# Performance work log

Measured on AMD Instinct MI355X. Metric: run time of the kernel, lower is better.

Reference implementation:

```python
import jax, jax.numpy as jnp
import numpy as np

B, O, E, H = 8192, 256, 64, 4  # batch, num_orbital, num_electron, hidden size


def setup_inputs() -> dict:
    key = jax.random.key(0)
    kx, k1, k2, k3, k4, k5, k6 = jax.random.split(key, 7)
    # occupancy vector: exactly E ones per sample among O orbitals
    perm_keys = jax.random.split(kx, B)
    occ = jax.vmap(lambda k: jax.random.permutation(k, O)[:E])(perm_keys)  # [B, E]
    x = jnp.zeros((B, O), jnp.float32).at[jnp.arange(B)[:, None], occ].set(1.0)
    # hidden Dense layers (kernel_init = uniform[0, 0.2), bias = zeros, as in flax default bias)
    W1 = jax.random.uniform(k1, (O, H), jnp.float32, 0.0, 0.2)
    b1 = jnp.zeros((H,), jnp.float32)
    W2 = jax.random.uniform(k2, (H, H), jnp.float32, 0.0, 0.2)
    b2 = jnp.zeros((H,), jnp.float32)
    # DenseGeneral: H -> (O, E); lecun_normal-ish init
    Wg = jax.random.normal(k3, (H, O, E), jnp.float32) / jnp.sqrt(jnp.float32(H))
    bg = jnp.zeros((O, E), jnp.float32)
    return {"x": x, "W1": W1, "b1": b1, "W2": W2, "b2": b2, "Wg": Wg, "bg": bg}


def reference(x, W1, b1, W2, b2, Wg, bg):
    # occupied orbital indices, ascending, fixed size E (vmapped jnp.nonzero)
    sel = jax.vmap(lambda row: jnp.nonzero(row, size=E, fill_value=0)[0])(x)  # [B, E] int
    # tiny MLP
    h = jax.nn.relu(x @ W1 + b1)        # [B, H]
    h = jax.nn.relu(h @ W2 + b2)        # [B, H]
    # DenseGeneral projection: [B, H] x [H, O, E] -> [B, O, E]
    M = jnp.einsum('bh,hoe->boe', h, Wg) + bg
    # gather occupied rows -> [B, E, E]
    rows = jnp.take_along_axis(M, sel[:, :, None], axis=1)
    return jnp.linalg.det(rows)          # [B]
```

## Files before the change

kernel.cpp:

```cpp
#include <hip/hip_runtime.h>

#define BB 8192
#define OO 256
#define EE 64
#define HH 4

__device__ __forceinline__ float bpermf(float v, int byte_idx) {
    return __int_as_float(__builtin_amdgcn_ds_bpermute(byte_idx, __float_as_int(v)));
}

__global__ __launch_bounds__(256) void backflow_det_reg(
    const float* __restrict__ x,  const float* __restrict__ W1,
    const float* __restrict__ b1, const float* __restrict__ W2,
    const float* __restrict__ b2, const float* __restrict__ Wg,
    const float* __restrict__ bg, float* __restrict__ out)
{
    __shared__ int sel_lds[4][EE];

    const int tid = threadIdx.x;
    const int tx  = tid & 63;
    const int w   = tid >> 6;
    const int b   = blockIdx.x * 4 + w;

    const float* xb = x + (size_t)b * OO;
    int base = 0;
    #pragma unroll
    for (int g = 0; g < 4; ++g) {
        const float xv = xb[g * 64 + tx];
        const unsigned long long m = __ballot(xv != 0.0f);
        if (xv != 0.0f) {
            const int pos = base + __popcll(m & ((1ull << tx) - 1ull));
            sel_lds[w][pos] = g * 64 + tx;
        }
        base += __popcll(m);
    }
    const int v_sel = sel_lds[w][tx];

    const float4 w1r = *reinterpret_cast<const float4*>(W1 + v_sel * HH);
    float s0 = w1r.x, s1 = w1r.y, s2 = w1r.z, s3 = w1r.w;
    #pragma unroll
    for (int d = 32; d >= 1; d >>= 1) {
        s0 += __shfl_xor(s0, d);
        s1 += __shfl_xor(s1, d);
        s2 += __shfl_xor(s2, d);
        s3 += __shfl_xor(s3, d);
    }
    const float h0 = fmaxf(s0 + b1[0], 0.0f);
    const float h1 = fmaxf(s1 + b1[1], 0.0f);
    const float h2 = fmaxf(s2 + b1[2], 0.0f);
    const float h3 = fmaxf(s3 + b1[3], 0.0f);
    float c[HH];
    #pragma unroll
    for (int j = 0; j < HH; ++j) {
        float t = b2[j];
        t = fmaf(h0, W2[0 * HH + j], t);
        t = fmaf(h1, W2[1 * HH + j], t);
        t = fmaf(h2, W2[2 * HH + j], t);
        t = fmaf(h3, W2[3 * HH + j], t);
        c[j] = fmaxf(t, 0.0f);
    }

    float a[EE];
    #pragma unroll
    for (int i = 0; i < EE; ++i) {
        const int si = __builtin_amdgcn_readlane(v_sel, i);
        float t = bg[si * EE + tx];
        t = fmaf(c[0], Wg[(0 * OO + si) * EE + tx], t);
        t = fmaf(c[1], Wg[(1 * OO + si) * EE + tx], t);
        t = fmaf(c[2], Wg[(2 * OO + si) * EE + tx], t);
        t = fmaf(c[3], Wg[(3 * OO + si) * EE + tx], t);
        a[i] = t;
    }

    double det_d = 1.0;
    #pragma unroll
    for (int k = 0; k < EE; ++k) {
        const int bidx = k << 2;
        const float pv  = bpermf(a[k], bidx);
        const float pvc = copysignf(fmaxf(fabsf(pv), 1e-20f), pv);
        det_d *= (double)pvc;
        const float ninv = -__builtin_amdgcn_rcpf(pvc);
        a[k] *= ninv;
        #pragma unroll
        for (int i = k + 1; i < EE; ++i) {
            const float m = bpermf(a[i], bidx);
            a[i] = fmaf(m, a[k], a[i]);
        }
    }
    if (tx == 0) {
        double dd = det_d;
        dd = fmin(dd, 3.0e38);
        dd = fmax(dd, -3.0e38);
        out[b] = (float)dd;
    }
}

extern "C" void kernel_launch(void* const* d_in, const int* in_sizes, int n_in,
                              void* d_out, int out_size, void* d_ws, size_t ws_size,
                              hipStream_t stream) {
    const float* x  = (const float*)d_in[0];
    const float* W1 = (const float*)d_in[1];
    const float* b1 = (const float*)d_in[2];
    const float* W2 = (const float*)d_in[3];
    const float* b2 = (const float*)d_in[4];
    const float* Wg = (const float*)d_in[5];
    const float* bg = (const float*)d_in[6];
    float* out = (float*)d_out;

    backflow_det_reg<<<dim3(BB / 4), dim3(256), 0, stream>>>(x, W1, b1, W2, b2, Wg, bg, out);
}
```

Baseline: 157.8 us.

## Pack two determinants per wavefront with two columns per lane

Each 64-lane wave now handles two samples: each half-wave of 32 lanes owns one matrix and each lane holds two adjacent columns as a float2. The Gaussian elimination is unchanged in structure, but each bpermute now serves two FMAs and the elimination count per sample is halved across lanes. This is meant to cut the cross-lane permute overhead per useful FMA and to enable packed FMA. In exchange the register footprint doubles to 128 floats per lane, which lowers occupancy, and the grid is halved.

```diff
diff --git a/kernel.cpp b/kernel.cpp
--- a/kernel.cpp
+++ b/kernel.cpp
@@ -5,41 +5,51 @@
 #define EE 64
 #define HH 4
 
-__device__ __forceinline__ float bpermf(float v, int byte_idx) {
-    return __int_as_float(__builtin_amdgcn_ds_bpermute(byte_idx, __float_as_int(v)));
+typedef float f32x2 __attribute__((ext_vector_type(2)));
+
+__device__ __forceinline__ float bpermf(int idx, float v) {
+    return __int_as_float(__builtin_amdgcn_ds_bpermute(idx, __float_as_int(v)));
 }
 
-__global__ __launch_bounds__(256) void backflow_det_reg(
+__global__ __launch_bounds__(256) void backflow_det_pk(
     const float* __restrict__ x,  const float* __restrict__ W1,
     const float* __restrict__ b1, const float* __restrict__ W2,
     const float* __restrict__ b2, const float* __restrict__ Wg,
     const float* __restrict__ bg, float* __restrict__ out)
 {
-    __shared__ int sel_lds[4][EE];
+    __shared__ int sel_lds[4][2][EE];
 
     const int tid = threadIdx.x;
     const int tx  = tid & 63;
     const int w   = tid >> 6;
-    const int b   = blockIdx.x * 4 + w;
+    const int l   = tx & 31;
+    const int hs  = tx >> 5;
+    const int b0  = (blockIdx.x * 4 + w) * 2;
 
-    const float* xb = x + (size_t)b * OO;
-    int base = 0;
     #pragma unroll
-    for (int g = 0; g < 4; ++g) {
-        const float xv = xb[g * 64 + tx];
-        const unsigned long long m = __ballot(xv != 0.0f);
-        if (xv != 0.0f) {
-            const int pos = base + __popcll(m & ((1ull << tx) - 1ull));
-            sel_lds[w][pos] = g * 64 + tx;
+    for (int s = 0; s < 2; ++s) {
+        const float* xb = x + (size_t)(b0 + s) * OO;
+        int base = 0;
+        #pragma unroll
+        for (int g = 0; g < 4; ++g) {
+            const float xv = xb[g * 64 + tx];
+            const unsigned long long m = __ballot(xv != 0.0f);
+            if (xv != 0.0f) {
+                const int pos = base + __popcll(m & ((1ull << tx) - 1ull));
+                sel_lds[w][s][pos] = g * 64 + tx;
+            }
+            base += __popcll(m);
         }
-        base += __popcll(m);
     }
-    const int v_sel = sel_lds[w][tx];
+    const int* selp = sel_lds[w][hs];
+    const int selLo = selp[l];
+    const int selHi = selp[l + 32];
 
-    const float4 w1r = *reinterpret_cast<const float4*>(W1 + v_sel * HH);
-    float s0 = w1r.x, s1 = w1r.y, s2 = w1r.z, s3 = w1r.w;
+    const float4 wa = *reinterpret_cast<const float4*>(W1 + selLo * HH);
+    const float4 wb = *reinterpret_cast<const float4*>(W1 + selHi * HH);
+    float s0 = wa.x + wb.x, s1 = wa.y + wb.y, s2 = wa.z + wb.z, s3 = wa.w + wb.w;
     #pragma unroll
-    for (int d = 32; d >= 1; d >>= 1) {
+    for (int d = 16; d >= 1; d >>= 1) {
         s0 += __shfl_xor(s0, d);
         s1 += __shfl_xor(s1, d);
         s2 += __shfl_xor(s2, d);
@@ -60,38 +70,44 @@
         c[j] = fmaxf(t, 0.0f);
     }
 
-    float a[EE];
+    const int col = l << 1;
+    f32x2 a[EE];
     #pragma unroll
     for (int i = 0; i < EE; ++i) {
-        const int si = __builtin_amdgcn_readlane(v_sel, i);
-        float t = bg[si * EE + tx];
-        t = fmaf(c[0], Wg[(0 * OO + si) * EE + tx], t);
-        t = fmaf(c[1], Wg[(1 * OO + si) * EE + tx], t);
-        t = fmaf(c[2], Wg[(2 * OO + si) * EE + tx], t);
-        t = fmaf(c[3], Wg[(3 * OO + si) * EE + tx], t);
+        const int si = selp[i];
+        f32x2 t = *reinterpret_cast<const f32x2*>(bg + si * EE + col);
+        #pragma unroll
+        for (int h = 0; h < HH; ++h) {
+            const f32x2 g2 = *reinterpret_cast<const f32x2*>(Wg + (h * OO + si) * EE + col);
+            t.x = fmaf(c[h], g2.x, t.x);
+            t.y = fmaf(c[h], g2.y, t.y);
+        }
         a[i] = t;
     }
 
+    const int bpb = (tx & 32) << 2;
     double det_d = 1.0;
     #pragma unroll
     for (int k = 0; k < EE; ++k) {
-        const int bidx = k << 2;
-        const float pv  = bpermf(a[k], bidx);
+        const int idx = bpb + ((k >> 1) << 2);
+        const float pv  = bpermf(idx, (k & 1) ? a[k].y : a[k].x);
         const float pvc = copysignf(fmaxf(fabsf(pv), 1e-20f), pv);
         det_d *= (double)pvc;
         const float ninv = -__builtin_amdgcn_rcpf(pvc);
-        a[k] *= ninv;
+        a[k].x *= ninv;
+        a[k].y *= ninv;
         #pragma unroll
         for (int i = k + 1; i < EE; ++i) {
-            const float m = bpermf(a[i], bidx);
-            a[i] = fmaf(m, a[k], a[i]);
+            const float m = bpermf(idx, (k & 1) ? a[i].y : a[i].x);
+            a[i].x = fmaf(m, a[k].x, a[i].x);
+            a[i].y = fmaf(m, a[k].y, a[i].y);
         }
     }
-    if (tx == 0) {
+    if (l == 0) {
         double dd = det_d;
         dd = fmin(dd, 3.0e38);
         dd = fmax(dd, -3.0e38);
-        out[b] = (float)dd;
+        out[b0 + hs] = (float)dd;
     }
 }
 
@@ -107,5 +123,5 @@
     const float* bg = (const float*)d_in[6];
     float* out = (float*)d_out;
 
-    backflow_det_reg<<<dim3(BB / 4), dim3(256), 0, stream>>>(x, W1, b1, W2, b2, Wg, bg, out);
+    backflow_det_pk<<<dim3(BB / 8), dim3(256), 0, stream>>>(x, W1, b1, W2, b2, Wg, bg, out);
 }
```

Measured after the change: 263.1 us. 66.7% more time.
